# Kernel tuning notes

Hardware: AMD Instinct MI355X
Metric: run time of the kernel (lower is better)

Reference implementation:

```python
import jax, jax.numpy as jnp
import numpy as np

DIM = 1024
HEADS = 16
SEEDS = 1
EPS = 1e-5

def _ln(x, g, b):
    mu = jnp.mean(x, axis=-1, keepdims=True)
    var = jnp.mean((x - mu) ** 2, axis=-1, keepdims=True)
    return (x - mu) * jax.lax.rsqrt(var + EPS) * g + b

def setup_inputs() -> dict:
    key = jax.random.key(0)
    ks = jax.random.split(key, 12)
    B, N = 32, 2048
    X = jax.random.normal(ks[0], (B, N, DIM), dtype=jnp.float32)
    mask = jax.random.randint(ks[1], (B, N), 0, 2, dtype=jnp.int32)
    s = 0.02
    return {
        "X": X,
        "mask": mask,
        "S": jax.random.normal(ks[2], (1, SEEDS, DIM), dtype=jnp.float32) * s,
        "Wq": jax.random.normal(ks[3], (DIM, DIM), dtype=jnp.float32) * s,
        "bq": jnp.zeros((DIM,), jnp.float32),
        "Wk": jax.random.normal(ks[4], (DIM, DIM), dtype=jnp.float32) * s,
        "bk": jnp.zeros((DIM,), jnp.float32),
        "Wv": jax.random.normal(ks[5], (DIM, DIM), dtype=jnp.float32) * s,
        "bv": jnp.zeros((DIM,), jnp.float32),
        "Wo": jax.random.normal(ks[6], (DIM, DIM), dtype=jnp.float32) * s,
        "bo": jnp.zeros((DIM,), jnp.float32),
        "g0": jnp.ones((DIM,), jnp.float32),
        "b0": jnp.zeros((DIM,), jnp.float32),
        "g1": jnp.ones((DIM,), jnp.float32),
        "b1": jnp.zeros((DIM,), jnp.float32),
    }

def reference(X, mask, S, Wq, bq, Wk, bk, Wv, bv, Wo, bo, g0, b0, g1, b1):
    B, N, _ = X.shape
    dh = DIM // HEADS
    Q = jnp.broadcast_to(S, (B, SEEDS, DIM))             # [B,S,D]
    Qp = (Q @ Wq.T + bq).reshape(B, SEEDS, HEADS, dh)    # split along channel dim == torch split/cat
    Kp = (X @ Wk.T + bk).reshape(B, N, HEADS, dh)
    Vp = (X @ Wv.T + bv).reshape(B, N, HEADS, dh)
    # NB: original scales by sqrt(dim_V), not sqrt(head_dim)
    score = jnp.einsum('bshd,bnhd->bhsn', Qp, Kp) / jnp.sqrt(jnp.float32(DIM))
    m = mask[:, None, None, :]                           # [B,1,1,N]
    score = jnp.where(m == 0, jnp.float32(-1e12), score)
    A = jax.nn.softmax(score, axis=-1) * m
    O = jnp.einsum('bhsn,bnhd->bshd', A, Vp).reshape(B, SEEDS, DIM)
    O = Q + O
    O = _ln(O, g0, b0)
    O = O + jax.nn.relu(O @ Wo.T + bo)
    O = _ln(O, g1, b1)
    return O[:, 0, :]  # num_seeds == 1 -> squeeze
```

## Files before the change

### kernel.cpp

```cpp
#include <hip/hip_runtime.h>
#include <hip/hip_bf16.h>
#include <cstdint>

#define DIM   1024
#define HEADS 16
#define BB    32
#define NN    2048
#define DH    64
#define PARTS 8
#define TS    32

constexpr float SCALE = 0.03125f;
constexpr float LN_EPS = 1e-5f;

typedef __attribute__((ext_vector_type(8))) short short8v;
typedef __attribute__((ext_vector_type(4))) short short4v;
typedef __attribute__((ext_vector_type(4))) float f32x4;

__device__ __forceinline__ short f2bf(float f) {
  union { __hip_bfloat16 h; short s; } u;
  u.h = __float2bfloat16(f);
  return u.s;
}
__device__ __forceinline__ float bf2f(short s) {
  union { unsigned int i; float f; } u;
  u.i = ((unsigned int)(unsigned short)s) << 16;
  return u.f;
}
__device__ __forceinline__ short8v pack8(float4 a, float4 b) {
  short8v v;
  v[0] = f2bf(a.x); v[1] = f2bf(a.y); v[2] = f2bf(a.z); v[3] = f2bf(a.w);
  v[4] = f2bf(b.x); v[5] = f2bf(b.y); v[6] = f2bf(b.z); v[7] = f2bf(b.w);
  return v;
}

__device__ __forceinline__ float block_sum256(float v, volatile float* red) {
  #pragma unroll
  for (int off = 32; off; off >>= 1) v += __shfl_xor(v, off);
  __syncthreads();
  if ((threadIdx.x & 63) == 0) red[threadIdx.x >> 6] = v;
  __syncthreads();
  return red[0] + red[1] + red[2] + red[3];
}

__global__ void k_front(const int* __restrict__ mask, const float* __restrict__ S,
                        const float* __restrict__ Wq, const float* __restrict__ bq,
                        const float* __restrict__ Wk, const float* __restrict__ bk,
                        short* __restrict__ qk_bf, float* __restrict__ qb,
                        int* __restrict__ idx, int* __restrict__ cnt) {
  __shared__ float qpl[DH];
  __shared__ int wsum[4];
  int tid = threadIdx.x;
  if (blockIdx.x >= 64) {
    int b = blockIdx.x - 64;
    const int* mb = mask + b * NN;
    int base = tid * 8;
    int loc[8], c = 0;
    #pragma unroll
    for (int i = 0; i < 8; ++i) { loc[i] = mb[base + i]; c += (loc[i] != 0); }
    int pre = c;
    #pragma unroll
    for (int off = 1; off < 64; off <<= 1) {
      int y = __shfl_up(pre, off);
      if ((tid & 63) >= off) pre += y;
    }
    if ((tid & 63) == 63) wsum[tid >> 6] = pre;
    __syncthreads();
    int wo = 0;
    for (int wv = 0; wv < (tid >> 6); ++wv) wo += wsum[wv];
    int pos = wo + pre - c;
    int* ib = idx + b * NN;
    #pragma unroll
    for (int i = 0; i < 8; ++i) if (loc[i]) ib[pos++] = base + i;
    if (tid == 255) cnt[b] = wo + pre;
    return;
  }
  int h = blockIdx.x >> 2, cblk = blockIdx.x & 3;
  int r = tid >> 2, j = tid & 3;
  int d = h * DH + r;
  const float* wr = Wq + (size_t)d * DIM + j * 256;
  const float* sp = S + j * 256;
  float a = 0.f;
  #pragma unroll 8
  for (int k = 0; k < 64; ++k) {
    float4 av = *(const float4*)(wr + k * 4);
    float4 sv = *(const float4*)(sp + k * 4);
    a += av.x * sv.x + av.y * sv.y + av.z * sv.z + av.w * sv.w;
  }
  a += __shfl_xor(a, 1);
  a += __shfl_xor(a, 2);
  if (j == 0) qpl[r] = a + bq[d];
  __syncthreads();
  if (cblk == 0 && tid < 64) {
    float v = qpl[tid] * bk[h * DH + tid];
    #pragma unroll
    for (int off = 32; off; off >>= 1) v += __shfl_xor(v, off);
    if (tid == 0) qb[h] = v;
  }
  int c = cblk * 256 + tid;
  float acc = 0.f;
  #pragma unroll 8
  for (int d0 = 0; d0 < DH; ++d0)
    acc += qpl[d0] * Wk[(size_t)(h * DH + d0) * DIM + c];
  int slot = (c >> 3) ^ (h & 7);
  qk_bf[h * 1024 + slot * 8 + (c & 7)] = f2bf(acc);
}

__global__ __launch_bounds__(512, 1) void k_fused3(const float* __restrict__ X,
                                                   const short* __restrict__ qk_bf,
                                                   const float* __restrict__ qb,
                                                   const int* __restrict__ idx,
                                                   const int* __restrict__ cnt,
                                                   short* __restrict__ Zt,
                                                   float* __restrict__ mt_g,
                                                   float* __restrict__ lt_g) {
  __shared__ short qlds[HEADS * 1024];
  __shared__ short xlds[TS * 1024];
  __shared__ short elbf[HEADS * 40];
  __shared__ short zst[HEADS * 1040];
  __shared__ float mt_l[32], lt_l[32], f_l[HEADS];
  __shared__ float mrun[2][HEADS], lrun[2][HEADS];
  int tid = threadIdx.x;
  int b = blockIdx.x >> 3, p = blockIdx.x & 7;
  int count = cnt[b];
  int chunk = (count + PARTS - 1) / PARTS;
  int pstart = p * chunk;
  int pend = pstart + chunk; if (pend > count) pend = count;
  int len = pend - pstart;
  int ntsub = (len + TS - 1) / TS;
  {
    const short8v* qg = (const short8v*)qk_bf;
    short8v* ql = (short8v*)qlds;
    #pragma unroll
    for (int i = 0; i < 4; ++i) ql[tid + i * 512] = qg[tid + i * 512];
  }
  if (tid < HEADS) { mrun[0][tid] = -3e38f; lrun[0][tid] = 0.f; }
  int wv = tid >> 6, lane = tid & 63;
  int r16 = lane & 15, kg = lane >> 4;
  int hx = r16 & 7;
  const int* ib = idx + b * NN;
  const float* Xb = X + (size_t)b * NN * DIM;
  const short* qrow = qlds + r16 * 1024;
  float qbv = qb[r16];
  int srow = wv * 16 + r16;
  int axor = (srow & 7) ^ (((srow >> 3) & 3) << 3);
  f32x4 acc[8];
  #pragma unroll
  for (int blk = 0; blk < 8; ++blk) acc[blk] = (f32x4){0.f, 0.f, 0.f, 0.f};
  float4 pfA[8], pfB[8];
  if (ntsub > 0) {
    #pragma unroll
    for (int k = 0; k < 8; ++k) {
      int i = tid + k * 512;
      int row = i >> 7, c8 = i & 127;
      int sl = pstart + row; if (sl >= pend) sl = pend - 1;
      int n = ib[sl];
      const float4* xg = (const float4*)(Xb + (size_t)n * DIM + c8 * 8);
      pfA[k] = xg[0]; pfB[k] = xg[1];
    }
  }
  __syncthreads();

  for (int t = 0; t < ntsub; ++t) {
    int tb = pstart + t * TS;
    int tpar = t & 1;
    __syncthreads();
    #pragma unroll
    for (int k = 0; k < 8; ++k) {
      int i = tid + k * 512;
      int row = i >> 7, c8 = i & 127;
      int sw = c8 ^ (row & 7) ^ ((row >> 3) << 3);
      *(short8v*)(xlds + row * 1024 + sw * 8) = pack8(pfA[k], pfB[k]);
    }
    __syncthreads();
    if (t + 1 < ntsub) {
      int tb1 = pstart + (t + 1) * TS;
      #pragma unroll
      for (int k = 0; k < 8; ++k) {
        int i = tid + k * 512;
        int row = i >> 7, c8 = i & 127;
        int sl = tb1 + row; if (sl >= pend) sl = pend - 1;
        int n = ib[sl];
        const float4* xg = (const float4*)(Xb + (size_t)n * DIM + c8 * 8);
        pfA[k] = xg[0]; pfB[k] = xg[1];
      }
    }
    float s_[4]; int vld[4];
    if (wv < 2) {
      const short* arow = xlds + srow * 1024;
      f32x4 qa = {0.f, 0.f, 0.f, 0.f};
      #pragma unroll 8
      for (int m = 0; m < 32; ++m) {
        int c8 = 4 * m + kg;
        short8v af = *(const short8v*)(arow + ((c8 ^ axor) << 3));
        short8v bf = *(const short8v*)(qrow + ((c8 ^ hx) << 3));
        qa = __builtin_amdgcn_mfma_f32_16x16x32_bf16(af, bf, qa, 0, 0, 0);
      }
      float mw = -3e38f;
      #pragma unroll
      for (int j = 0; j < 4; ++j) {
        int slot = tb + wv * 16 + kg * 4 + j;
        vld[j] = slot < pend;
        s_[j] = vld[j] ? (qa[j] + qbv) * SCALE : -3e38f;
        mw = fmaxf(mw, s_[j]);
      }
      mw = fmaxf(mw, __shfl_xor(mw, 16));
      mw = fmaxf(mw, __shfl_xor(mw, 32));
      if (kg == 0) mt_l[wv * 16 + r16] = mw;
    }
    __syncthreads();
    if (wv < 2) {
      float m_t = fmaxf(mt_l[r16], mt_l[16 + r16]);
      float mo = mrun[tpar][r16];
      float mn = fmaxf(mo, m_t);
      float es = 0.f;
      #pragma unroll
      for (int j = 0; j < 4; ++j) {
        float e = vld[j] ? __expf(s_[j] - mn) : 0.f;
        elbf[r16 * 40 + (wv * 16 + kg * 4 + j)] = f2bf(e);
        es += e;
      }
      es += __shfl_xor(es, 16);
      es += __shfl_xor(es, 32);
      if (kg == 0) lt_l[wv * 16 + r16] = es;
      if (tid < 16) {
        f_l[tid] = __expf(mo - mn);
        mrun[tpar ^ 1][tid] = mn;
      }
    }
    __syncthreads();
    {
      int g = kg;
      float fj0 = f_l[g * 4 + 0], fj1 = f_l[g * 4 + 1];
      float fj2 = f_l[g * 4 + 2], fj3 = f_l[g * 4 + 3];
      #pragma unroll
      for (int blk = 0; blk < 8; ++blk) {
        acc[blk][0] *= fj0; acc[blk][1] *= fj1;
        acc[blk][2] *= fj2; acc[blk][3] *= fj3;
      }
      short8v ea = *(const short8v*)(elbf + r16 * 40 + g * 8);
      #pragma unroll
      for (int blk = 0; blk < 8; ++blk) {
        int c = wv * 128 + blk * 16 + r16;
        int ch = c >> 3, cl = c & 7;
        short8v xb;
        #pragma unroll
        for (int u = 0; u < 8; ++u) {
          int s = g * 8 + u;
          int sw = ch ^ (s & 7) ^ ((s >> 3) << 3);
          xb[u] = xlds[s * 1024 + sw * 8 + cl];
        }
        acc[blk] = __builtin_amdgcn_mfma_f32_16x16x32_bf16(ea, xb, acc[blk], 0, 0, 0);
      }
      if (tid < 16)
        lrun[tpar ^ 1][tid] = lrun[tpar][tid] * f_l[tid] + lt_l[tid] + lt_l[16 + tid];
    }
  }
  int par = ntsub & 1;
  if (tid < 16) {
    mt_g[(b * PARTS + p) * HEADS + tid] = mrun[par][tid];
    lt_g[(b * PARTS + p) * HEADS + tid] = lrun[par][tid];
  }
  #pragma unroll
  for (int blk = 0; blk < 8; ++blk) {
    int c = wv * 128 + blk * 16 + r16;
    #pragma unroll
    for (int j = 0; j < 4; ++j)
      zst[(kg * 4 + j) * 1040 + c] = f2bf(acc[blk][j]);
  }
  __syncthreads();
  short* zbase = Zt + ((size_t)(b * PARTS + p) * HEADS) * DIM;
  #pragma unroll
  for (int it = 0; it < 8; ++it) {
    int e4 = it * 2048 + tid * 4;
    int h = e4 >> 10, c = e4 & 1023;
    *(short4v*)(zbase + h * DIM + c) = *(const short4v*)(zst + h * 1040 + c);
  }
}

__global__ __launch_bounds__(256) void k_tov(const short* __restrict__ Zt,
                                             const float* __restrict__ mt_g,
                                             const float* __restrict__ lt_g,
                                             const float* __restrict__ Wv,
                                             float* __restrict__ T,
                                             float* __restrict__ lsum) {
  int b = blockIdx.x >> 4, h = blockIdx.x & 15;
  int tid = threadIdx.x;
  __shared__ float zlds[DIM];
  float m_b = -3e38f;
  #pragma unroll
  for (int t = 0; t < PARTS; ++t)
    m_b = fmaxf(m_b, mt_g[(b * PARTS + t) * HEADS + h]);
  float L = 0.f;
  #pragma unroll
  for (int t = 0; t < PARTS; ++t) {
    float lt = lt_g[(b * PARTS + t) * HEADS + h];
    if (lt > 0.f) L += lt * __expf(mt_g[(b * PARTS + t) * HEADS + h] - m_b);
  }
  float inv = L > 0.f ? 1.f / L : 0.f;
  float4 zs = make_float4(0.f, 0.f, 0.f, 0.f);
  #pragma unroll
  for (int t = 0; t < PARTS; ++t) {
    float lt = lt_g[(b * PARTS + t) * HEADS + h];
    if (lt <= 0.f) continue;
    float f = __expf(mt_g[(b * PARTS + t) * HEADS + h] - m_b) * inv;
    short4v z4 = *(const short4v*)(Zt + ((size_t)(b * PARTS + t) * HEADS + h) * DIM + tid * 4);
    zs.x += f * bf2f(z4[0]); zs.y += f * bf2f(z4[1]);
    zs.z += f * bf2f(z4[2]); zs.w += f * bf2f(z4[3]);
  }
  *(float4*)(zlds + tid * 4) = zs;
  __syncthreads();
  int wv = tid >> 6, lane = tid & 63;
  float4 zr[4];
  #pragma unroll
  for (int j = 0; j < 4; ++j) zr[j] = *(const float4*)(zlds + lane * 4 + j * 256);
  for (int i = 0; i < 16; ++i) {
    int df = h * 64 + wv * 16 + i;
    const float* wr = Wv + (size_t)df * DIM + lane * 4;
    float a = 0.f;
    #pragma unroll
    for (int j = 0; j < 4; ++j) {
      float4 w4 = *(const float4*)(wr + j * 256);
      a += zr[j].x * w4.x + zr[j].y * w4.y + zr[j].z * w4.z + zr[j].w * w4.w;
    }
    #pragma unroll
    for (int off = 32; off; off >>= 1) a += __shfl_xor(a, off);
    if (lane == 0) T[(size_t)b * DIM + df] = a;
  }
  if (tid == 0) lsum[b * HEADS + h] = L > 0.f ? 1.f : 0.f;
}

__global__ void k_ln0(const float* __restrict__ S, const float* __restrict__ T,
                      const float* __restrict__ lsum, const float* __restrict__ bv,
                      const float* __restrict__ g0, const float* __restrict__ b0,
                      float* __restrict__ U) {
  __shared__ float red[4];
  int b = blockIdx.x, tid = threadIdx.x, d0 = tid * 4;
  float4 s4 = *(const float4*)(S + d0);
  float4 t4 = *(const float4*)(T + (size_t)b * DIM + d0);
  float4 v4 = *(const float4*)(bv + d0);
  float lh = lsum[b * HEADS + (d0 >> 6)];
  float x0 = s4.x + t4.x + lh * v4.x;
  float x1 = s4.y + t4.y + lh * v4.y;
  float x2 = s4.z + t4.z + lh * v4.z;
  float x3 = s4.w + t4.w + lh * v4.w;
  float mu = block_sum256(x0 + x1 + x2 + x3, red) * (1.f / DIM);
  float e0 = x0 - mu, e1 = x1 - mu, e2 = x2 - mu, e3 = x3 - mu;
  float var = block_sum256(e0 * e0 + e1 * e1 + e2 * e2 + e3 * e3, red) * (1.f / DIM);
  float r = rsqrtf(var + LN_EPS);
  float4 g4 = *(const float4*)(g0 + d0);
  float4 bb4 = *(const float4*)(b0 + d0);
  float4 o;
  o.x = e0 * r * g4.x + bb4.x;
  o.y = e1 * r * g4.y + bb4.y;
  o.z = e2 * r * g4.z + bb4.z;
  o.w = e3 * r * g4.w + bb4.w;
  *(float4*)(U + (size_t)b * DIM + d0) = o;
}

__global__ void k_wo(const float* __restrict__ U, const float* __restrict__ Wo,
                     const float* __restrict__ bo, float* __restrict__ R) {
  int wave = threadIdx.x >> 6, lane = threadIdx.x & 63;
  int dfb = blockIdx.x;
  for (int dot = wave; dot < 128; dot += 4) {
    int b = dot >> 2, dfl = dot & 3;
    int df = dfb * 4 + dfl;
    const float* wr = Wo + (size_t)df * DIM + lane * 4;
    const float* ur = U + (size_t)b * DIM + lane * 4;
    float acc = 0.f;
    #pragma unroll
    for (int k = 0; k < 4; ++k) {
      float4 a = *(const float4*)(wr + k * 256);
      float4 u = *(const float4*)(ur + k * 256);
      acc += a.x * u.x + a.y * u.y + a.z * u.z + a.w * u.w;
    }
    #pragma unroll
    for (int off = 32; off; off >>= 1) acc += __shfl_xor(acc, off);
    if (lane == 0) R[(size_t)b * DIM + df] = fmaxf(acc + bo[df], 0.f);
  }
}

__global__ void k_ln1(const float* __restrict__ U, const float* __restrict__ R,
                      const float* __restrict__ g1, const float* __restrict__ b1,
                      float* __restrict__ out) {
  __shared__ float red[4];
  int b = blockIdx.x, tid = threadIdx.x, d0 = tid * 4;
  float4 u4 = *(const float4*)(U + (size_t)b * DIM + d0);
  float4 r4 = *(const float4*)(R + (size_t)b * DIM + d0);
  float x0 = u4.x + r4.x, x1 = u4.y + r4.y, x2 = u4.z + r4.z, x3 = u4.w + r4.w;
  float mu = block_sum256(x0 + x1 + x2 + x3, red) * (1.f / DIM);
  float e0 = x0 - mu, e1 = x1 - mu, e2 = x2 - mu, e3 = x3 - mu;
  float var = block_sum256(e0 * e0 + e1 * e1 + e2 * e2 + e3 * e3, red) * (1.f / DIM);
  float r = rsqrtf(var + LN_EPS);
  float4 g4 = *(const float4*)(g1 + d0);
  float4 bb4 = *(const float4*)(b1 + d0);
  float4 o;
  o.x = e0 * r * g4.x + bb4.x;
  o.y = e1 * r * g4.y + bb4.y;
  o.z = e2 * r * g4.z + bb4.z;
  o.w = e3 * r * g4.w + bb4.w;
  *(float4*)(out + (size_t)b * DIM + d0) = o;
}

extern "C" void kernel_launch(void* const* d_in, const int* in_sizes, int n_in,
                              void* d_out, int out_size, void* d_ws, size_t ws_size,
                              hipStream_t stream) {
  (void)in_sizes; (void)n_in; (void)out_size; (void)ws_size;
  const float* X  = (const float*)d_in[0];
  const int*   mask = (const int*)d_in[1];
  const float* S  = (const float*)d_in[2];
  const float* Wq = (const float*)d_in[3];
  const float* bq = (const float*)d_in[4];
  const float* Wk = (const float*)d_in[5];
  const float* bk = (const float*)d_in[6];
  const float* Wv = (const float*)d_in[7];
  const float* bv = (const float*)d_in[8];
  const float* Wo = (const float*)d_in[9];
  const float* bo = (const float*)d_in[10];
  const float* g0 = (const float*)d_in[11];
  const float* b0 = (const float*)d_in[12];
  const float* g1 = (const float*)d_in[13];
  const float* b1 = (const float*)d_in[14];
  float* out = (float*)d_out;

  char* base  = (char*)d_ws;
  size_t off = 0;
  short* Zt   = (short*)(base + off); off += (size_t)BB * PARTS * HEADS * DIM * 2;
  short* qkbf = (short*)(base + off); off += HEADS * 1024 * 2;
  float* qb   = (float*)(base + off); off += 64;
  float* mt   = (float*)(base + off); off += (size_t)BB * PARTS * HEADS * 4;
  float* lt   = (float*)(base + off); off += (size_t)BB * PARTS * HEADS * 4;
  float* lsum = (float*)(base + off); off += BB * HEADS * 4;
  int*   idx  = (int*)(base + off);   off += (size_t)BB * NN * 4;
  int*   cnt  = (int*)(base + off);   off += 256;
  float* T    = (float*)(base + off); off += (size_t)BB * DIM * 4;
  float* U    = (float*)(base + off); off += (size_t)BB * DIM * 4;
  float* R    = (float*)(base + off); off += (size_t)BB * DIM * 4;

  k_front  <<<96,  256, 0, stream>>>(mask, S, Wq, bq, Wk, bk, qkbf, qb, idx, cnt);
  k_fused3 <<<256, 512, 0, stream>>>(X, qkbf, qb, idx, cnt, Zt, mt, lt);
  k_tov    <<<512, 256, 0, stream>>>(Zt, mt, lt, Wv, T, lsum);
  k_ln0    <<<32,  256, 0, stream>>>(S, T, lsum, bv, g0, b0, U);
  k_wo     <<<256, 256, 0, stream>>>(U, Wo, bo, R);
  k_ln1    <<<32,  256, 0, stream>>>(U, R, g1, b1, out);
}
```

Measured before the change: 93.85 us.

## Split score MFMA across all waves, fuse LN0 into tov, split front

The score MFMA in the fused attention kernel is now split along K across all 8 waves rather than run on 2 waves, with partial results reduced through shared memory. This removes one barrier-separated max pass. LayerNorm0 is folded into the tov kernel: a per-batch atomic counter lets the last head block do the normalisation, which drops one launch. The Wq projection moves into a separate, wider-parallel front kernel. This adds one launch and a global round trip for Qp, in exchange for a shorter per-block serial dot product.

```diff
diff --git a/kernel.cpp b/kernel.cpp
--- a/kernel.cpp
+++ b/kernel.cpp
@@ -43,16 +43,15 @@
   return red[0] + red[1] + red[2] + red[3];
 }
 
-__global__ void k_front(const int* __restrict__ mask, const float* __restrict__ S,
-                        const float* __restrict__ Wq, const float* __restrict__ bq,
-                        const float* __restrict__ Wk, const float* __restrict__ bk,
-                        short* __restrict__ qk_bf, float* __restrict__ qb,
-                        int* __restrict__ idx, int* __restrict__ cnt) {
-  __shared__ float qpl[DH];
+__global__ void k_front1(const int* __restrict__ mask, const float* __restrict__ S,
+                         const float* __restrict__ Wq, const float* __restrict__ bq,
+                         float* __restrict__ Qp, int* __restrict__ idx,
+                         int* __restrict__ cnt, int* __restrict__ cntB) {
   __shared__ int wsum[4];
   int tid = threadIdx.x;
-  if (blockIdx.x >= 64) {
-    int b = blockIdx.x - 64;
+  if (blockIdx.x < 32) {
+    int b = blockIdx.x;
+    if (tid == 0) cntB[b] = 0;
     const int* mb = mask + b * NN;
     int base = tid * 8;
     int loc[8], c = 0;
@@ -75,21 +74,30 @@
     if (tid == 255) cnt[b] = wo + pre;
     return;
   }
+  int q = blockIdx.x - 32;
+  int rgrp = tid >> 5, l32 = tid & 31;
+  int d = q * 8 + rgrp;
+  const float* wr = Wq + (size_t)d * DIM + l32 * 4;
+  const float* sp = S + l32 * 4;
+  float a = 0.f;
+  #pragma unroll
+  for (int k = 0; k < 8; ++k) {
+    float4 av = *(const float4*)(wr + k * 128);
+    float4 sv = *(const float4*)(sp + k * 128);
+    a += av.x * sv.x + av.y * sv.y + av.z * sv.z + av.w * sv.w;
+  }
+  #pragma unroll
+  for (int off = 16; off; off >>= 1) a += __shfl_xor(a, off);
+  if (l32 == 0) Qp[d] = a + bq[d];
+}
+
+__global__ void k_front2(const float* __restrict__ Qp, const float* __restrict__ Wk,
+                         const float* __restrict__ bk, short* __restrict__ qk_bf,
+                         float* __restrict__ qb) {
+  __shared__ float qpl[DH];
+  int tid = threadIdx.x;
   int h = blockIdx.x >> 2, cblk = blockIdx.x & 3;
-  int r = tid >> 2, j = tid & 3;
-  int d = h * DH + r;
-  const float* wr = Wq + (size_t)d * DIM + j * 256;
-  const float* sp = S + j * 256;
-  float a = 0.f;
-  #pragma unroll 8
-  for (int k = 0; k < 64; ++k) {
-    float4 av = *(const float4*)(wr + k * 4);
-    float4 sv = *(const float4*)(sp + k * 4);
-    a += av.x * sv.x + av.y * sv.y + av.z * sv.z + av.w * sv.w;
-  }
-  a += __shfl_xor(a, 1);
-  a += __shfl_xor(a, 2);
-  if (j == 0) qpl[r] = a + bq[d];
+  if (tid < DH) qpl[tid] = Qp[h * DH + tid];
   __syncthreads();
   if (cblk == 0 && tid < 64) {
     float v = qpl[tid] * bk[h * DH + tid];
@@ -106,7 +114,7 @@
   qk_bf[h * 1024 + slot * 8 + (c & 7)] = f2bf(acc);
 }
 
-__global__ __launch_bounds__(512, 1) void k_fused3(const float* __restrict__ X,
+__global__ __launch_bounds__(512, 1) void k_fused4(const float* __restrict__ X,
                                                    const short* __restrict__ qk_bf,
                                                    const float* __restrict__ qb,
                                                    const int* __restrict__ idx,
@@ -116,10 +124,11 @@
                                                    float* __restrict__ lt_g) {
   __shared__ short qlds[HEADS * 1024];
   __shared__ short xlds[TS * 1024];
-  __shared__ short elbf[HEADS * 40];
-  __shared__ short zst[HEADS * 1040];
-  __shared__ float mt_l[32], lt_l[32], f_l[HEADS];
+  __shared__ __align__(16) short elbf[HEADS * 40];
+  __shared__ __align__(16) short zst[HEADS * 1040];
+  __shared__ float lt_l[32], f_l[HEADS];
   __shared__ float mrun[2][HEADS], lrun[2][HEADS];
+  float* pacc = (float*)zst;
   int tid = threadIdx.x;
   int b = blockIdx.x >> 3, p = blockIdx.x & 7;
   int count = cnt[b];
@@ -142,8 +151,10 @@
   const float* Xb = X + (size_t)b * NN * DIM;
   const short* qrow = qlds + r16 * 1024;
   float qbv = qb[r16];
-  int srow = wv * 16 + r16;
-  int axor = (srow & 7) ^ (((srow >> 3) & 3) << 3);
+  int sh = wv >> 2, kq = wv & 3;
+  int srow = sh * 16 + r16;
+  int ax = (srow & 7) ^ (((srow >> 3) & 3) << 3);
+  const short* arow = xlds + srow * 1024;
   f32x4 acc[8];
   #pragma unroll
   for (int blk = 0; blk < 8; ++blk) acc[blk] = (f32x4){0.f, 0.f, 0.f, 0.f};
@@ -185,44 +196,51 @@
         pfA[k] = xg[0]; pfB[k] = xg[1];
       }
     }
-    float s_[4]; int vld[4];
-    if (wv < 2) {
-      const short* arow = xlds + srow * 1024;
+    {
       f32x4 qa = {0.f, 0.f, 0.f, 0.f};
-      #pragma unroll 8
-      for (int m = 0; m < 32; ++m) {
-        int c8 = 4 * m + kg;
-        short8v af = *(const short8v*)(arow + ((c8 ^ axor) << 3));
+      #pragma unroll
+      for (int m = 0; m < 8; ++m) {
+        int c8 = kq * 32 + m * 4 + kg;
+        short8v af = *(const short8v*)(arow + ((c8 ^ ax) << 3));
         short8v bf = *(const short8v*)(qrow + ((c8 ^ hx) << 3));
         qa = __builtin_amdgcn_mfma_f32_16x16x32_bf16(af, bf, qa, 0, 0, 0);
       }
+      *(f32x4*)(pacc + (wv * 64 + lane) * 4) = qa;
+    }
+    __syncthreads();
+    if ((wv & 3) == 0) {
+      int oh = sh ^ 1;
+      f32x4 own = {0.f, 0.f, 0.f, 0.f}, oth = {0.f, 0.f, 0.f, 0.f};
+      #pragma unroll
+      for (int q = 0; q < 4; ++q) {
+        own += *(const f32x4*)(pacc + ((sh * 4 + q) * 64 + lane) * 4);
+        oth += *(const f32x4*)(pacc + ((oh * 4 + q) * 64 + lane) * 4);
+      }
+      float s_[4];
       float mw = -3e38f;
       #pragma unroll
       for (int j = 0; j < 4; ++j) {
-        int slot = tb + wv * 16 + kg * 4 + j;
-        vld[j] = slot < pend;
-        s_[j] = vld[j] ? (qa[j] + qbv) * SCALE : -3e38f;
+        int so = tb + sh * 16 + kg * 4 + j;
+        s_[j] = (so < pend) ? (own[j] + qbv) * SCALE : -3e38f;
         mw = fmaxf(mw, s_[j]);
+        int so2 = tb + oh * 16 + kg * 4 + j;
+        float s2 = (so2 < pend) ? (oth[j] + qbv) * SCALE : -3e38f;
+        mw = fmaxf(mw, s2);
       }
       mw = fmaxf(mw, __shfl_xor(mw, 16));
       mw = fmaxf(mw, __shfl_xor(mw, 32));
-      if (kg == 0) mt_l[wv * 16 + r16] = mw;
-    }
-    __syncthreads();
-    if (wv < 2) {
-      float m_t = fmaxf(mt_l[r16], mt_l[16 + r16]);
       float mo = mrun[tpar][r16];
-      float mn = fmaxf(mo, m_t);
+      float mn = fmaxf(mo, mw);
       float es = 0.f;
       #pragma unroll
       for (int j = 0; j < 4; ++j) {
-        float e = vld[j] ? __expf(s_[j] - mn) : 0.f;
-        elbf[r16 * 40 + (wv * 16 + kg * 4 + j)] = f2bf(e);
+        float e = (s_[j] > -1e30f) ? __expf(s_[j] - mn) : 0.f;
+        elbf[r16 * 40 + (sh * 16 + kg * 4 + j)] = f2bf(e);
         es += e;
       }
       es += __shfl_xor(es, 16);
       es += __shfl_xor(es, 32);
-      if (kg == 0) lt_l[wv * 16 + r16] = es;
+      if (kg == 0) lt_l[sh * 16 + r16] = es;
       if (tid < 16) {
         f_l[tid] = __expf(mo - mn);
         mrun[tpar ^ 1][tid] = mn;
@@ -261,6 +279,7 @@
     mt_g[(b * PARTS + p) * HEADS + tid] = mrun[par][tid];
     lt_g[(b * PARTS + p) * HEADS + tid] = lrun[par][tid];
   }
+  __syncthreads();
   #pragma unroll
   for (int blk = 0; blk < 8; ++blk) {
     int c = wv * 128 + blk * 16 + r16;
@@ -278,15 +297,23 @@
   }
 }
 
-__global__ __launch_bounds__(256) void k_tov(const short* __restrict__ Zt,
-                                             const float* __restrict__ mt_g,
-                                             const float* __restrict__ lt_g,
-                                             const float* __restrict__ Wv,
-                                             float* __restrict__ T,
-                                             float* __restrict__ lsum) {
+__global__ __launch_bounds__(256) void k_tov2(const short* __restrict__ Zt,
+                                              const float* __restrict__ mt_g,
+                                              const float* __restrict__ lt_g,
+                                              const float* __restrict__ Wv,
+                                              const float* __restrict__ S,
+                                              const float* __restrict__ bv,
+                                              const float* __restrict__ g0,
+                                              const float* __restrict__ b0,
+                                              float* __restrict__ T,
+                                              float* __restrict__ lsum,
+                                              float* __restrict__ U,
+                                              int* __restrict__ cntB) {
   int b = blockIdx.x >> 4, h = blockIdx.x & 15;
   int tid = threadIdx.x;
   __shared__ float zlds[DIM];
+  __shared__ float red[4];
+  __shared__ int last;
   float m_b = -3e38f;
   #pragma unroll
   for (int t = 0; t < PARTS; ++t)
@@ -309,6 +336,7 @@
     zs.z += f * bf2f(z4[2]); zs.w += f * bf2f(z4[3]);
   }
   *(float4*)(zlds + tid * 4) = zs;
+  if (tid == 0) lsum[b * HEADS + h] = L > 0.f ? 1.f : 0.f;
   __syncthreads();
   int wv = tid >> 6, lane = tid & 63;
   float4 zr[4];
@@ -327,35 +355,36 @@
     for (int off = 32; off; off >>= 1) a += __shfl_xor(a, off);
     if (lane == 0) T[(size_t)b * DIM + df] = a;
   }
-  if (tid == 0) lsum[b * HEADS + h] = L > 0.f ? 1.f : 0.f;
-}
-
-__global__ void k_ln0(const float* __restrict__ S, const float* __restrict__ T,
-                      const float* __restrict__ lsum, const float* __restrict__ bv,
-                      const float* __restrict__ g0, const float* __restrict__ b0,
-                      float* __restrict__ U) {
-  __shared__ float red[4];
-  int b = blockIdx.x, tid = threadIdx.x, d0 = tid * 4;
-  float4 s4 = *(const float4*)(S + d0);
-  float4 t4 = *(const float4*)(T + (size_t)b * DIM + d0);
-  float4 v4 = *(const float4*)(bv + d0);
-  float lh = lsum[b * HEADS + (d0 >> 6)];
-  float x0 = s4.x + t4.x + lh * v4.x;
-  float x1 = s4.y + t4.y + lh * v4.y;
-  float x2 = s4.z + t4.z + lh * v4.z;
-  float x3 = s4.w + t4.w + lh * v4.w;
-  float mu = block_sum256(x0 + x1 + x2 + x3, red) * (1.f / DIM);
-  float e0 = x0 - mu, e1 = x1 - mu, e2 = x2 - mu, e3 = x3 - mu;
-  float var = block_sum256(e0 * e0 + e1 * e1 + e2 * e2 + e3 * e3, red) * (1.f / DIM);
-  float r = rsqrtf(var + LN_EPS);
-  float4 g4 = *(const float4*)(g0 + d0);
-  float4 bb4 = *(const float4*)(b0 + d0);
-  float4 o;
-  o.x = e0 * r * g4.x + bb4.x;
-  o.y = e1 * r * g4.y + bb4.y;
-  o.z = e2 * r * g4.z + bb4.z;
-  o.w = e3 * r * g4.w + bb4.w;
-  *(float4*)(U + (size_t)b * DIM + d0) = o;
+  __syncthreads();
+  if (tid == 0) {
+    __threadfence();
+    last = (atomicAdd(&cntB[b], 1) == HEADS - 1);
+  }
+  __syncthreads();
+  if (last) {
+    __threadfence();
+    int d0 = tid * 4;
+    float4 s4 = *(const float4*)(S + d0);
+    float4 t4 = *(const float4*)(T + (size_t)b * DIM + d0);
+    float4 v4 = *(const float4*)(bv + d0);
+    float lh = lsum[b * HEADS + (d0 >> 6)];
+    float x0 = s4.x + t4.x + lh * v4.x;
+    float x1 = s4.y + t4.y + lh * v4.y;
+    float x2 = s4.z + t4.z + lh * v4.z;
+    float x3 = s4.w + t4.w + lh * v4.w;
+    float mu = block_sum256(x0 + x1 + x2 + x3, red) * (1.f / DIM);
+    float e0 = x0 - mu, e1 = x1 - mu, e2 = x2 - mu, e3 = x3 - mu;
+    float var = block_sum256(e0 * e0 + e1 * e1 + e2 * e2 + e3 * e3, red) * (1.f / DIM);
+    float r = rsqrtf(var + LN_EPS);
+    float4 g4 = *(const float4*)(g0 + d0);
+    float4 bb4 = *(const float4*)(b0 + d0);
+    float4 o;
+    o.x = e0 * r * g4.x + bb4.x;
+    o.y = e1 * r * g4.y + bb4.y;
+    o.z = e2 * r * g4.z + bb4.z;
+    o.w = e3 * r * g4.w + bb4.w;
+    *(float4*)(U + (size_t)b * DIM + d0) = o;
+  }
 }
 
 __global__ void k_wo(const float* __restrict__ U, const float* __restrict__ Wo,
@@ -433,14 +462,16 @@
   float* lsum = (float*)(base + off); off += BB * HEADS * 4;
   int*   idx  = (int*)(base + off);   off += (size_t)BB * NN * 4;
   int*   cnt  = (int*)(base + off);   off += 256;
+  int*   cntB = (int*)(base + off);   off += 256;
+  float* Qp   = (float*)(base + off); off += DIM * 4;
   float* T    = (float*)(base + off); off += (size_t)BB * DIM * 4;
   float* U    = (float*)(base + off); off += (size_t)BB * DIM * 4;
   float* R    = (float*)(base + off); off += (size_t)BB * DIM * 4;
 
-  k_front  <<<96,  256, 0, stream>>>(mask, S, Wq, bq, Wk, bk, qkbf, qb, idx, cnt);
-  k_fused3 <<<256, 512, 0, stream>>>(X, qkbf, qb, idx, cnt, Zt, mt, lt);
-  k_tov    <<<512, 256, 0, stream>>>(Zt, mt, lt, Wv, T, lsum);
-  k_ln0    <<<32,  256, 0, stream>>>(S, T, lsum, bv, g0, b0, U);
+  k_front1 <<<160, 256, 0, stream>>>(mask, S, Wq, bq, Qp, idx, cnt, cntB);
+  k_front2 <<<64,  256, 0, stream>>>(Qp, Wk, bk, qkbf, qb);
+  k_fused4 <<<256, 512, 0, stream>>>(X, qkbf, qb, idx, cnt, Zt, mt, lt);
+  k_tov2   <<<512, 256, 0, stream>>>(Zt, mt, lt, Wv, S, bv, g0, b0, T, lsum, U, cntB);
   k_wo     <<<256, 256, 0, stream>>>(U, Wo, bo, R);
   k_ln1    <<<32,  256, 0, stream>>>(U, R, g1, b1, out);
 }
```

Measured after the change: 101.4 us. 8.1% more time.
